# Kernel optimization log

Hardware: AMD Instinct MI355X
Metric: run time of the kernel (lower is better)

The kernel has to match this reference:

```python
import jax, jax.numpy as jnp
import numpy as np

D_MODEL = 1024
N_HEADS = 16
D_K = D_MODEL // N_HEADS


def setup_inputs() -> dict:
    key = jax.random.key(0)
    ks = jax.random.split(key, 5)
    x = jax.random.normal(ks[0], (4, 2048, D_MODEL), dtype=jnp.float32)
    # nn.Linear stores weight as [out, in]; we store transposed [in, out] for x @ W
    w_qkv = jax.random.normal(ks[1], (D_MODEL, 3 * D_MODEL), dtype=jnp.float32) / np.sqrt(D_MODEL)
    b_qkv = jnp.zeros((3 * D_MODEL,), dtype=jnp.float32)
    w_fc = jax.random.normal(ks[2], (D_MODEL, D_MODEL), dtype=jnp.float32) / np.sqrt(D_MODEL)
    b_fc = jnp.zeros((D_MODEL,), dtype=jnp.float32)
    ln_g = jnp.ones((D_MODEL,), dtype=jnp.float32)
    ln_b = jnp.zeros((D_MODEL,), dtype=jnp.float32)
    return {"x": x, "w_qkv": w_qkv, "b_qkv": b_qkv, "w_fc": w_fc, "b_fc": b_fc,
            "ln_g": ln_g, "ln_b": ln_b}


def _layernorm(x, g, b, eps=1e-5):
    mu = jnp.mean(x, axis=-1, keepdims=True)
    var = jnp.mean(jnp.square(x - mu), axis=-1, keepdims=True)
    return (x - mu) * jax.lax.rsqrt(var + eps) * g + b


def reference(x, w_qkv, b_qkv, w_fc, b_fc, ln_g, ln_b):
    residual = x
    xn = _layernorm(x, ln_g, ln_b)
    B, L, D = xn.shape
    qkv = xn @ w_qkv + b_qkv  # [B, L, 3D]
    q, k, v = jnp.split(qkv, 3, axis=-1)
    # b l (h d) -> b h l d
    def to_heads(t):
        return t.reshape(B, L, N_HEADS, D_K).transpose(0, 2, 1, 3)
    q, k, v = to_heads(q), to_heads(k), to_heads(v)
    scale = 1.0 / np.sqrt(D_K)
    scores = jnp.einsum('bhld,bhmd->bhlm', q, k) * scale  # [B,H,L,L]
    attn = jax.nn.softmax(scores, axis=-1)
    # dropout is identity in eval mode
    out = jnp.einsum('bhlm,bhmd->bhld', attn, v)  # [B,H,L,d]
    out = out.transpose(0, 2, 1, 3).reshape(B, L, D)  # b h l d -> b l (h d)
    out = out @ w_fc + b_fc
    return out + residual
```

## Files before the change

kernel.cpp:

```cpp
#include <hip/hip_runtime.h>
#include <hip/hip_bf16.h>
#include <cstdint>
#include <cstddef>

using bf16 = __hip_bfloat16;
typedef __attribute__((ext_vector_type(4))) float f32x4;
typedef __attribute__((ext_vector_type(8))) short bf16x8;

#define D_MODEL 1024
#define SEQ     2048
#define NB      4
#define NHEAD   16
#define DHEAD   64
#define NROWS   (NB * SEQ)

__device__ __forceinline__ void load_lds16(const void* g, void* l) {
  __builtin_amdgcn_global_load_lds(
      (const __attribute__((address_space(1))) unsigned int*)g,
      (__attribute__((address_space(3))) unsigned int*)l, 16, 0, 0);
}

__device__ __forceinline__ unsigned short f2bf(float f) {
  bf16 h = __float2bfloat16(f);
  return *(unsigned short*)&h;
}

__device__ __forceinline__ unsigned pk_trunc(float a, float b) {
  union { float f; unsigned u; } ca, cb;
  ca.f = a; cb.f = b;
  return (ca.u >> 16) | (cb.u & 0xffff0000u);
}

__global__ __launch_bounds__(256) void ln_kernel(
    const float* __restrict__ x, const float* __restrict__ g,
    const float* __restrict__ bb, bf16* __restrict__ xn) {
  int row  = blockIdx.x * 4 + (threadIdx.x >> 6);
  int lane = threadIdx.x & 63;
  const float4* xr = (const float4*)(x + (size_t)row * D_MODEL);
  float v[16], s = 0.f;
#pragma unroll
  for (int i = 0; i < 4; i++) {
    float4 t = xr[lane + 64 * i];
    v[4 * i] = t.x; v[4 * i + 1] = t.y; v[4 * i + 2] = t.z; v[4 * i + 3] = t.w;
    s += t.x + t.y + t.z + t.w;
  }
#pragma unroll
  for (int off = 32; off; off >>= 1) s += __shfl_xor(s, off, 64);
  float mean = s * (1.f / D_MODEL);
  float vs = 0.f;
#pragma unroll
  for (int i = 0; i < 16; i++) { float d = v[i] - mean; vs += d * d; }
#pragma unroll
  for (int off = 32; off; off >>= 1) vs += __shfl_xor(vs, off, 64);
  float rstd = rsqrtf(vs * (1.f / D_MODEL) + 1e-5f);
  ushort4* op = (ushort4*)(xn + (size_t)row * D_MODEL);
#pragma unroll
  for (int i = 0; i < 4; i++) {
    float4 gv = ((const float4*)g)[lane + 64 * i];
    float4 bv = ((const float4*)bb)[lane + 64 * i];
    ushort4 o;
    o.x = f2bf((v[4 * i]     - mean) * rstd * gv.x + bv.x);
    o.y = f2bf((v[4 * i + 1] - mean) * rstd * gv.y + bv.y);
    o.z = f2bf((v[4 * i + 2] - mean) * rstd * gv.z + bv.z);
    o.w = f2bf((v[4 * i + 3] - mean) * rstd * gv.w + bv.w);
    op[lane + 64 * i] = o;
  }
}

__global__ __launch_bounds__(256) void transpose_kernel(
    const float* __restrict__ w_qkv, bf16* __restrict__ wqkvT,
    const float* __restrict__ w_fc, bf16* __restrict__ wfcT) {
  __shared__ float tile[32][33];
  const float* in; bf16* out; int C, c0;
  if (blockIdx.x < 96) { in = w_qkv; out = wqkvT; C = 3072; c0 = blockIdx.x * 32; }
  else                 { in = w_fc;  out = wfcT;  C = 1024; c0 = (blockIdx.x - 96) * 32; }
  int r0 = blockIdx.y * 32;
  int tx = threadIdx.x & 31, ty = threadIdx.x >> 5;
  for (int i = ty; i < 32; i += 8)
    tile[i][tx] = in[(size_t)(r0 + i) * C + c0 + tx];
  __syncthreads();
  for (int i = ty; i < 32; i += 8)
    out[(size_t)(c0 + i) * 1024 + r0 + tx] = __float2bfloat16(tile[tx][i]);
}

__device__ __forceinline__ void store_ct(bf16* p, float v)  { *p = __float2bfloat16(v); }
__device__ __forceinline__ void store_ct(float* p, float v) { *p = v; }

template <int SPLIT, int RESID, typename CT>
__global__ __launch_bounds__(256) void gemm_bt(
    const bf16* __restrict__ A, const bf16* __restrict__ Bt,
    const float* __restrict__ bias, const float* __restrict__ resid,
    CT* __restrict__ C, bf16* __restrict__ vt, int M, int N, int K) {
  __shared__ __attribute__((aligned(16))) bf16 Alds[128 * 64];
  __shared__ __attribute__((aligned(16))) bf16 Blds[128 * 64];
  int tid = threadIdx.x, wave = tid >> 6, lane = tid & 63;
  int ntiles = N >> 7;
  int bm = blockIdx.x / ntiles, bn = blockIdx.x % ntiles;
  int m0 = bm << 7, n0 = bn << 7;
  int wm = (wave >> 1) << 6, wn = (wave & 1) << 6;
  int srow = tid >> 3;
  int sw8  = (((tid & 7) ^ (srow & 7)) << 3);
  int frow = lane & 15, quad = lane >> 4;
  const bf16* Ap[4];
  const bf16* Bp[4];
#pragma unroll
  for (int s = 0; s < 4; s++) {
    Ap[s] = A  + (size_t)(m0 + s * 32 + srow) * K + sw8;
    Bp[s] = Bt + (size_t)(n0 + s * 32 + srow) * K + sw8;
  }
  f32x4 acc[4][4] = {};
  for (int k0 = 0; k0 < K; k0 += 64) {
    __syncthreads();
#pragma unroll
    for (int s = 0; s < 4; s++) {
      load_lds16(Ap[s], (char*)Alds + s * 4096 + tid * 16);
      load_lds16(Bp[s], (char*)Blds + s * 4096 + tid * 16);
      Ap[s] += 64; Bp[s] += 64;
    }
    __syncthreads();
    bf16x8 af[4][2], bv[4][2];
#pragma unroll
    for (int i = 0; i < 4; i++)
#pragma unroll
      for (int kk = 0; kk < 2; kk++) {
        int e = (((kk * 4 + quad) ^ (frow & 7)) << 3);
        af[i][kk] = *(const bf16x8*)&Alds[(wm + i * 16 + frow) * 64 + e];
        bv[i][kk] = *(const bf16x8*)&Blds[(wn + i * 16 + frow) * 64 + e];
      }
#pragma unroll
    for (int i = 0; i < 4; i++)
#pragma unroll
      for (int j = 0; j < 4; j++) {
        acc[i][j] = __builtin_amdgcn_mfma_f32_16x16x32_bf16(af[i][0], bv[j][0], acc[i][j], 0, 0, 0);
        acc[i][j] = __builtin_amdgcn_mfma_f32_16x16x32_bf16(af[i][1], bv[j][1], acc[i][j], 0, 0, 0);
      }
  }
#pragma unroll
  for (int i = 0; i < 4; i++) {
    int row0 = m0 + wm + i * 16 + (quad << 2);
#pragma unroll
    for (int j = 0; j < 4; j++) {
      int col = n0 + wn + j * 16 + frow;
      float bvs = bias[col];
      if (SPLIT && col >= 2048) {
        int hd = col - 2048;
        int b = row0 >> 11, seq0 = row0 & 2047;
        int within = seq0 & 63, mt = within >> 4, q4 = (within >> 2) & 3;
        int pos = (seq0 & ~63) + ((mt >> 1) << 5) + (q4 << 3) + ((mt & 1) << 2);
        ushort4 pk;
        pk.x = f2bf(acc[i][j][0] + bvs);
        pk.y = f2bf(acc[i][j][1] + bvs);
        pk.z = f2bf(acc[i][j][2] + bvs);
        pk.w = f2bf(acc[i][j][3] + bvs);
        *(ushort4*)&vt[((size_t)(b * 1024 + hd)) * SEQ + pos] = pk;
      } else {
        int stride = SPLIT ? 2048 : N;
        float scale = (SPLIT && col < 1024) ? 0.18033688f : 1.0f;
#pragma unroll
        for (int r = 0; r < 4; r++) {
          size_t idx = (size_t)(row0 + r) * stride + col;
          float val = (acc[i][j][r] + bvs) * scale;
          if (RESID) val += resid[idx];
          store_ct(&C[idx], val);
        }
      }
    }
  }
}


template <bool STG>
__device__ __forceinline__ void ktile_qkv(
    const bf16* Aw, const bf16* Bw,
    bf16* Ad, bf16* Bd,
    const bf16* const* Ab, const bf16* const* Bb, size_t koff,
    int tid, int frow, int e_lo, int e_hi, f32x4 (&acc)[8][3]) {
  __builtin_amdgcn_sched_barrier(0);
  bf16x8 bv[3][2];
#pragma unroll
  for (int j = 0; j < 3; j++) {
    bv[j][0] = *(const bf16x8*)&Bw[(j * 16 + frow) * 64 + e_lo];
    bv[j][1] = *(const bf16x8*)&Bw[(j * 16 + frow) * 64 + e_hi];
  }
  bf16x8 a00 = *(const bf16x8*)&Aw[(frow) * 64 + e_lo];
  bf16x8 a01 = *(const bf16x8*)&Aw[(frow) * 64 + e_hi];
  bf16x8 a10 = *(const bf16x8*)&Aw[(16 + frow) * 64 + e_lo];
  bf16x8 a11 = *(const bf16x8*)&Aw[(16 + frow) * 64 + e_hi];
  if (STG) {
#pragma unroll
    for (int u = 0; u < 4; u++)
      load_lds16(Ab[u] + koff, (char*)Ad + u * 8192 + tid * 16);
#pragma unroll
    for (int u = 0; u < 3; u++)
      load_lds16(Bb[u] + koff, (char*)Bd + u * 8192 + tid * 16);
  }
  __builtin_amdgcn_s_barrier();
  asm volatile("s_waitcnt lgkmcnt(0)" ::: "memory");
  __builtin_amdgcn_sched_barrier(0);
  __builtin_amdgcn_s_setprio(1);
#pragma unroll
  for (int j = 0; j < 3; j++) {
    acc[0][j] = __builtin_amdgcn_mfma_f32_16x16x32_bf16(a00, bv[j][0], acc[0][j], 0, 0, 0);
    acc[0][j] = __builtin_amdgcn_mfma_f32_16x16x32_bf16(a01, bv[j][1], acc[0][j], 0, 0, 0);
    acc[1][j] = __builtin_amdgcn_mfma_f32_16x16x32_bf16(a10, bv[j][0], acc[1][j], 0, 0, 0);
    acc[1][j] = __builtin_amdgcn_mfma_f32_16x16x32_bf16(a11, bv[j][1], acc[1][j], 0, 0, 0);
  }
  __builtin_amdgcn_s_setprio(0);
  __builtin_amdgcn_s_barrier();
#pragma unroll
  for (int p = 1; p < 4; p++) {
    bf16x8 c00 = *(const bf16x8*)&Aw[((2 * p) * 16 + frow) * 64 + e_lo];
    bf16x8 c01 = *(const bf16x8*)&Aw[((2 * p) * 16 + frow) * 64 + e_hi];
    bf16x8 c10 = *(const bf16x8*)&Aw[((2 * p + 1) * 16 + frow) * 64 + e_lo];
    bf16x8 c11 = *(const bf16x8*)&Aw[((2 * p + 1) * 16 + frow) * 64 + e_hi];
    __builtin_amdgcn_s_barrier();
    asm volatile("s_waitcnt lgkmcnt(0)" ::: "memory");
    __builtin_amdgcn_sched_barrier(0);
    __builtin_amdgcn_s_setprio(1);
#pragma unroll
    for (int j = 0; j < 3; j++) {
      acc[2 * p][j]     = __builtin_amdgcn_mfma_f32_16x16x32_bf16(c00, bv[j][0], acc[2 * p][j], 0, 0, 0);
      acc[2 * p][j]     = __builtin_amdgcn_mfma_f32_16x16x32_bf16(c01, bv[j][1], acc[2 * p][j], 0, 0, 0);
      acc[2 * p + 1][j] = __builtin_amdgcn_mfma_f32_16x16x32_bf16(c10, bv[j][0], acc[2 * p + 1][j], 0, 0, 0);
      acc[2 * p + 1][j] = __builtin_amdgcn_mfma_f32_16x16x32_bf16(c11, bv[j][1], acc[2 * p + 1][j], 0, 0, 0);
    }
    __builtin_amdgcn_s_setprio(0);
    if (p == 3) {
      asm volatile("s_waitcnt vmcnt(0)" ::: "memory");
      __builtin_amdgcn_sched_barrier(0);
    }
    __builtin_amdgcn_s_barrier();
  }
}

__global__ __launch_bounds__(512, 2) void gemm256_qkv(
    const bf16* __restrict__ A, const bf16* __restrict__ Bt,
    const float* __restrict__ bias, bf16* __restrict__ C, bf16* __restrict__ vt) {
  __shared__ __attribute__((aligned(16))) bf16 AL0[256 * 64];
  __shared__ __attribute__((aligned(16))) bf16 AL1[256 * 64];
  __shared__ __attribute__((aligned(16))) bf16 BL0[192 * 64];
  __shared__ __attribute__((aligned(16))) bf16 BL1[192 * 64];

  int bid = blockIdx.x;
  int logical = (bid & 7) * 64 + (bid >> 3);
  int bm = logical >> 4;
  int bn = logical & 15;
  int m0 = bm * 256, n0 = bn * 192;

  int tid = threadIdx.x, wave = tid >> 6, lane = tid & 63;
  int wm = (wave >> 2) * 128;
  int wn = (wave & 3) * 48;
  int srow = tid >> 3;
  int sw8 = (((tid & 7) ^ (srow & 7)) << 3);
  int frow = lane & 15, quad = lane >> 4;
  int e_lo = ((quad ^ (frow & 7)) << 3);
  int e_hi = (((4 + quad) ^ (frow & 7)) << 3);

  const bf16* Ab[4];
  const bf16* Bb[3];
#pragma unroll
  for (int u = 0; u < 4; u++) Ab[u] = A + (size_t)(m0 + u * 64 + srow) * 1024 + sw8;
#pragma unroll
  for (int u = 0; u < 3; u++) Bb[u] = Bt + (size_t)(n0 + u * 64 + srow) * 1024 + sw8;

#pragma unroll
  for (int u = 0; u < 4; u++) load_lds16(Ab[u], (char*)AL0 + u * 8192 + tid * 16);
#pragma unroll
  for (int u = 0; u < 3; u++) load_lds16(Bb[u], (char*)BL0 + u * 8192 + tid * 16);
  asm volatile("s_waitcnt vmcnt(0)" ::: "memory");
  __builtin_amdgcn_sched_barrier(0);
  __builtin_amdgcn_s_barrier();

  f32x4 acc[8][3] = {};
  const bf16* A0w = AL0 + wm * 64;
  const bf16* B0w = BL0 + wn * 64;
  const bf16* A1w = AL1 + wm * 64;
  const bf16* B1w = BL1 + wn * 64;

  size_t ko = 64;
#pragma unroll 1
  for (int t2 = 0; t2 < 14; t2 += 2) {
    ktile_qkv<true>(A0w, B0w, AL1, BL1, Ab, Bb, ko,      tid, frow, e_lo, e_hi, acc);
    ktile_qkv<true>(A1w, B1w, AL0, BL0, Ab, Bb, ko + 64, tid, frow, e_lo, e_hi, acc);
    ko += 128;
  }
  ktile_qkv<true >(A0w, B0w, AL1, BL1, Ab, Bb, ko, tid, frow, e_lo, e_hi, acc);
  ktile_qkv<false>(A1w, B1w, AL0, BL0, Ab, Bb, 0,  tid, frow, e_lo, e_hi, acc);

#pragma unroll
  for (int i = 0; i < 8; i++) {
    int row0 = m0 + wm + i * 16 + (quad << 2);
#pragma unroll
    for (int j = 0; j < 3; j++) {
      int col = n0 + wn + j * 16 + frow;
      float bvs = bias[col];
      if (col >= 2048) {
        int hd = col - 2048;
        int b = row0 >> 11, seq0 = row0 & 2047;
        int within = seq0 & 63, mt = within >> 4, q4 = (within >> 2) & 3;
        int pos = (seq0 & ~63) + ((mt >> 1) << 5) + (q4 << 3) + ((mt & 1) << 2);
        ushort4 pk;
        pk.x = f2bf(acc[i][j][0] + bvs);
        pk.y = f2bf(acc[i][j][1] + bvs);
        pk.z = f2bf(acc[i][j][2] + bvs);
        pk.w = f2bf(acc[i][j][3] + bvs);
        *(ushort4*)&vt[((size_t)(b * 1024 + hd)) * SEQ + pos] = pk;
      } else {
        float scale = (col < 1024) ? 0.18033688f : 1.0f;
#pragma unroll
        for (int r = 0; r < 4; r++) {
          size_t idx = (size_t)(row0 + r) * 2048 + col;
          C[idx] = __float2bfloat16((acc[i][j][r] + bvs) * scale);
        }
      }
    }
  }
}


__device__ __forceinline__ void stage_kv(
    const bf16* Kp0, const bf16* Kp1, const bf16* Vp0, const bf16* Vp1,
    bf16* KB, bf16* VB, int tid) {
  load_lds16(Kp0, (char*)KB + tid * 16);
  load_lds16(Kp1, (char*)KB + 4096 + tid * 16);
  load_lds16(Vp0, (char*)VB + tid * 16);
  load_lds16(Vp1, (char*)VB + 4096 + tid * 16);
}

__device__ __forceinline__ void kv_tile(
    const bf16* KL, const bf16* VL, int frow, int e0,
    const bf16x8 (&qf)[2][2], f32x4 (&l4)[2], f32x4 (&o)[4][2]) {
  f32x4 s[4][2] = {};
#pragma unroll
  for (int mt = 0; mt < 4; mt++) {
    bf16x8 af0 = *(const bf16x8*)&KL[(mt * 16 + frow) * 64 + e0];
    bf16x8 af1 = *(const bf16x8*)&KL[(mt * 16 + frow) * 64 + (e0 ^ 32)];
#pragma unroll
    for (int qt2 = 0; qt2 < 2; qt2++) {
      s[mt][qt2] = __builtin_amdgcn_mfma_f32_16x16x32_bf16(af0, qf[qt2][0], s[mt][qt2], 0, 0, 0);
      s[mt][qt2] = __builtin_amdgcn_mfma_f32_16x16x32_bf16(af1, qf[qt2][1], s[mt][qt2], 0, 0, 0);
    }
  }
  uint2 pk[2][4];
#pragma unroll
  for (int qt2 = 0; qt2 < 2; qt2++)
#pragma unroll
    for (int mt = 0; mt < 4; mt++) {
      f32x4 pv;
      pv[0] = __builtin_amdgcn_exp2f(s[mt][qt2][0]);
      pv[1] = __builtin_amdgcn_exp2f(s[mt][qt2][1]);
      pv[2] = __builtin_amdgcn_exp2f(s[mt][qt2][2]);
      pv[3] = __builtin_amdgcn_exp2f(s[mt][qt2][3]);
      l4[qt2] += pv;
      pk[qt2][mt].x = pk_trunc(pv[0], pv[1]);
      pk[qt2][mt].y = pk_trunc(pv[2], pv[3]);
    }
#pragma unroll
  for (int dt = 0; dt < 4; dt++) {
    bf16x8 vf0 = *(const bf16x8*)&VL[(dt * 16 + frow) * 64 + e0];
    bf16x8 vf1 = *(const bf16x8*)&VL[(dt * 16 + frow) * 64 + (e0 ^ 32)];
#pragma unroll
    for (int qt2 = 0; qt2 < 2; qt2++) {
      union { unsigned u[4]; bf16x8 v; } pf0, pf1;
      pf0.u[0] = pk[qt2][0].x; pf0.u[1] = pk[qt2][0].y;
      pf0.u[2] = pk[qt2][1].x; pf0.u[3] = pk[qt2][1].y;
      pf1.u[0] = pk[qt2][2].x; pf1.u[1] = pk[qt2][2].y;
      pf1.u[2] = pk[qt2][3].x; pf1.u[3] = pk[qt2][3].y;
      o[dt][qt2] = __builtin_amdgcn_mfma_f32_16x16x32_bf16(vf0, pf0.v, o[dt][qt2], 0, 0, 0);
      o[dt][qt2] = __builtin_amdgcn_mfma_f32_16x16x32_bf16(vf1, pf1.v, o[dt][qt2], 0, 0, 0);
    }
  }
}

__global__ __launch_bounds__(256, 4) void attn_kernel(
    const bf16* __restrict__ qk, const bf16* __restrict__ vt,
    bf16* __restrict__ aout) {
  int bh = blockIdx.x;
  int qt = blockIdx.y;
  int bb = bh >> 4, h = bh & 15;
  const bf16* Qg = qk + (size_t)bb * SEQ * 2048 + h * DHEAD;
  const bf16* Kg = Qg + D_MODEL;
  const bf16* Vg = vt + (size_t)bh * DHEAD * SEQ;

  __shared__ __attribute__((aligned(16))) bf16 Qlds[128 * 64];
  __shared__ __attribute__((aligned(16))) bf16 Klds[64 * 64];
  __shared__ __attribute__((aligned(16))) bf16 Vlds[64 * 64];

  int tid = threadIdx.x, wave = tid >> 6, lane = tid & 63;
  int prow = tid >> 3, pch = tid & 7;
  int lch8 = ((pch ^ (prow & 7)) << 3);
  int frow = lane & 15, quad = lane >> 4;
  int e0 = ((quad ^ (frow & 7)) << 3);
  int q0 = qt * 128;

  bf16* K0 = Klds;  bf16* V0 = Vlds;
  bf16* K1 = Qlds;  bf16* V1 = Qlds + 64 * 64;

  const bf16* Kp0 = Kg + (size_t)prow * 2048 + lch8;
  const bf16* Kp1 = Kg + (size_t)(32 + prow) * 2048 + lch8;
  const bf16* Vp0 = Vg + (size_t)prow * SEQ + lch8;
  const bf16* Vp1 = Vg + (size_t)(32 + prow) * SEQ + lch8;
  const size_t KT = (size_t)1 << 17;

#pragma unroll
  for (int s2 = 0; s2 < 4; s2++)
    load_lds16(Qg + (size_t)(q0 + s2 * 32 + prow) * 2048 + lch8,
               (char*)Qlds + s2 * 4096 + tid * 16);
  __syncthreads();
  bf16x8 qf[2][2];
#pragma unroll
  for (int qt2 = 0; qt2 < 2; qt2++)
#pragma unroll
    for (int kk = 0; kk < 2; kk++)
      qf[qt2][kk] =
          *(const bf16x8*)&Qlds[(wave * 32 + qt2 * 16 + frow) * 64 + (e0 ^ (kk * 32))];
  stage_kv(Kp0, Kp1, Vp0, Vp1, K0, V0, tid);
  __syncthreads();

  f32x4 l4[2] = {};
  f32x4 o[4][2] = {};

#pragma unroll 1
  for (int kt = 0; kt < 30; kt += 2) {
    stage_kv(Kp0 + KT, Kp1 + KT, Vp0 + 64, Vp1 + 64, K1, V1, tid);
    kv_tile(K0, V0, frow, e0, qf, l4, o);
    __syncthreads();
    stage_kv(Kp0 + 2 * KT, Kp1 + 2 * KT, Vp0 + 128, Vp1 + 128, K0, V0, tid);
    kv_tile(K1, V1, frow, e0, qf, l4, o);
    __syncthreads();
    Kp0 += 2 * KT; Kp1 += 2 * KT; Vp0 += 128; Vp1 += 128;
  }
  stage_kv(Kp0 + KT, Kp1 + KT, Vp0 + 64, Vp1 + 64, K1, V1, tid);
  kv_tile(K0, V0, frow, e0, qf, l4, o);
  __syncthreads();
  kv_tile(K1, V1, frow, e0, qf, l4, o);

  float linv[2];
#pragma unroll
  for (int qt2 = 0; qt2 < 2; qt2++) {
    float v = (l4[qt2][0] + l4[qt2][1]) + (l4[qt2][2] + l4[qt2][3]);
    v += __shfl_xor(v, 16, 64);
    v += __shfl_xor(v, 32, 64);
    linv[qt2] = 1.f / v;
  }

  __syncthreads();
  bf16* Tw = (wave == 0) ? Qlds
           : (wave == 1) ? Qlds + 32 * 80
           : (wave == 2) ? Klds : Vlds;
#pragma unroll
  for (int qt2 = 0; qt2 < 2; qt2++)
#pragma unroll
    for (int dt = 0; dt < 4; dt++) {
      ushort4 pk;
      pk.x = f2bf(o[dt][qt2][0] * linv[qt2]);
      pk.y = f2bf(o[dt][qt2][1] * linv[qt2]);
      pk.z = f2bf(o[dt][qt2][2] * linv[qt2]);
      pk.w = f2bf(o[dt][qt2][3] * linv[qt2]);
      *(ushort4*)&Tw[(qt2 * 16 + frow) * 80 + dt * 16 + quad * 4] = pk;
    }
  int rq = lane >> 1, d0 = (lane & 1) * 32;
  size_t grow = (size_t)(bb * SEQ + q0 + wave * 32 + rq);
#pragma unroll
  for (int i = 0; i < 4; i++) {
    bf16x8 v8 = *(const bf16x8*)&Tw[rq * 80 + d0 + i * 8];
    *(bf16x8*)&aout[grow * D_MODEL + h * DHEAD + d0 + i * 8] = v8;
  }
}

extern "C" void kernel_launch(void* const* d_in, const int* in_sizes, int n_in,
                              void* d_out, int out_size, void* d_ws, size_t ws_size,
                              hipStream_t stream) {
  const float* x     = (const float*)d_in[0];
  const float* w_qkv = (const float*)d_in[1];
  const float* b_qkv = (const float*)d_in[2];
  const float* w_fc  = (const float*)d_in[3];
  const float* b_fc  = (const float*)d_in[4];
  const float* ln_g  = (const float*)d_in[5];
  const float* ln_b  = (const float*)d_in[6];
  float* out = (float*)d_out;

  char* ws = (char*)d_ws;
  bf16* xn    = (bf16*)(ws);
  bf16* wqkvT = (bf16*)(ws + (16u << 20));
  bf16* wfcT  = (bf16*)(ws + (22u << 20));
  bf16* qk    = (bf16*)(ws + (24u << 20));
  bf16* vt    = (bf16*)(ws + (56u << 20));
  bf16* aout  = (bf16*)(ws);

  ln_kernel<<<NROWS / 4, 256, 0, stream>>>(x, ln_g, ln_b, xn);
  transpose_kernel<<<dim3(128, 32), 256, 0, stream>>>(w_qkv, wqkvT, w_fc, wfcT);
  gemm256_qkv<<<512, 512, 0, stream>>>(xn, wqkvT, b_qkv, qk, vt);
  attn_kernel<<<dim3(NB * NHEAD, SEQ / 128), 256, 0, stream>>>(qk, vt, aout);
  gemm_bt<0, 1, float><<<(NROWS / 128) * (D_MODEL / 128), 256, 0, stream>>>(
      aout, wfcT, b_fc, x, out, nullptr, NROWS, D_MODEL, D_MODEL);
}
```

Before: 270.7 us.

## Replace FC GEMM with 8-wave double-buffered kernel and split QKV staging waits

The simple single-buffered 128x128 output-projection GEMM is replaced by a 512-thread, 256x128-tile kernel. It reuses the templated double-buffered k-tile routine from the QKV GEMM, with an XCD-aware block remap. The shared k-tile routine now issues half of the A-tile prefetch mid-tile and uses partial vmcnt waits instead of a full drain, so global-to-LDS loads overlap more with MFMA work. This risks incorrect synchronisation if the vmcnt counts do not match the load ordering. The FC grid also shrinks to 256 blocks, which may leave CUs underused.

```diff
diff --git a/kernel.cpp b/kernel.cpp
--- a/kernel.cpp
+++ b/kernel.cpp
@@ -83,102 +83,16 @@
     out[(size_t)(c0 + i) * 1024 + r0 + tx] = __float2bfloat16(tile[tx][i]);
 }
 
-__device__ __forceinline__ void store_ct(bf16* p, float v)  { *p = __float2bfloat16(v); }
-__device__ __forceinline__ void store_ct(float* p, float v) { *p = v; }
-
-template <int SPLIT, int RESID, typename CT>
-__global__ __launch_bounds__(256) void gemm_bt(
-    const bf16* __restrict__ A, const bf16* __restrict__ Bt,
-    const float* __restrict__ bias, const float* __restrict__ resid,
-    CT* __restrict__ C, bf16* __restrict__ vt, int M, int N, int K) {
-  __shared__ __attribute__((aligned(16))) bf16 Alds[128 * 64];
-  __shared__ __attribute__((aligned(16))) bf16 Blds[128 * 64];
-  int tid = threadIdx.x, wave = tid >> 6, lane = tid & 63;
-  int ntiles = N >> 7;
-  int bm = blockIdx.x / ntiles, bn = blockIdx.x % ntiles;
-  int m0 = bm << 7, n0 = bn << 7;
-  int wm = (wave >> 1) << 6, wn = (wave & 1) << 6;
-  int srow = tid >> 3;
-  int sw8  = (((tid & 7) ^ (srow & 7)) << 3);
-  int frow = lane & 15, quad = lane >> 4;
-  const bf16* Ap[4];
-  const bf16* Bp[4];
-#pragma unroll
-  for (int s = 0; s < 4; s++) {
-    Ap[s] = A  + (size_t)(m0 + s * 32 + srow) * K + sw8;
-    Bp[s] = Bt + (size_t)(n0 + s * 32 + srow) * K + sw8;
-  }
-  f32x4 acc[4][4] = {};
-  for (int k0 = 0; k0 < K; k0 += 64) {
-    __syncthreads();
-#pragma unroll
-    for (int s = 0; s < 4; s++) {
-      load_lds16(Ap[s], (char*)Alds + s * 4096 + tid * 16);
-      load_lds16(Bp[s], (char*)Blds + s * 4096 + tid * 16);
-      Ap[s] += 64; Bp[s] += 64;
-    }
-    __syncthreads();
-    bf16x8 af[4][2], bv[4][2];
-#pragma unroll
-    for (int i = 0; i < 4; i++)
-#pragma unroll
-      for (int kk = 0; kk < 2; kk++) {
-        int e = (((kk * 4 + quad) ^ (frow & 7)) << 3);
-        af[i][kk] = *(const bf16x8*)&Alds[(wm + i * 16 + frow) * 64 + e];
-        bv[i][kk] = *(const bf16x8*)&Blds[(wn + i * 16 + frow) * 64 + e];
-      }
-#pragma unroll
-    for (int i = 0; i < 4; i++)
-#pragma unroll
-      for (int j = 0; j < 4; j++) {
-        acc[i][j] = __builtin_amdgcn_mfma_f32_16x16x32_bf16(af[i][0], bv[j][0], acc[i][j], 0, 0, 0);
-        acc[i][j] = __builtin_amdgcn_mfma_f32_16x16x32_bf16(af[i][1], bv[j][1], acc[i][j], 0, 0, 0);
-      }
-  }
-#pragma unroll
-  for (int i = 0; i < 4; i++) {
-    int row0 = m0 + wm + i * 16 + (quad << 2);
-#pragma unroll
-    for (int j = 0; j < 4; j++) {
-      int col = n0 + wn + j * 16 + frow;
-      float bvs = bias[col];
-      if (SPLIT && col >= 2048) {
-        int hd = col - 2048;
-        int b = row0 >> 11, seq0 = row0 & 2047;
-        int within = seq0 & 63, mt = within >> 4, q4 = (within >> 2) & 3;
-        int pos = (seq0 & ~63) + ((mt >> 1) << 5) + (q4 << 3) + ((mt & 1) << 2);
-        ushort4 pk;
-        pk.x = f2bf(acc[i][j][0] + bvs);
-        pk.y = f2bf(acc[i][j][1] + bvs);
-        pk.z = f2bf(acc[i][j][2] + bvs);
-        pk.w = f2bf(acc[i][j][3] + bvs);
-        *(ushort4*)&vt[((size_t)(b * 1024 + hd)) * SEQ + pos] = pk;
-      } else {
-        int stride = SPLIT ? 2048 : N;
-        float scale = (SPLIT && col < 1024) ? 0.18033688f : 1.0f;
-#pragma unroll
-        for (int r = 0; r < 4; r++) {
-          size_t idx = (size_t)(row0 + r) * stride + col;
-          float val = (acc[i][j][r] + bvs) * scale;
-          if (RESID) val += resid[idx];
-          store_ct(&C[idx], val);
-        }
-      }
-    }
-  }
-}
-
-
-template <bool STG>
-__device__ __forceinline__ void ktile_qkv(
+template <int BCH, bool STG, bool LAST>
+__device__ __forceinline__ void ktile8(
     const bf16* Aw, const bf16* Bw,
     bf16* Ad, bf16* Bd,
-    const bf16* const* Ab, const bf16* const* Bb, size_t koff,
-    int tid, int frow, int e_lo, int e_hi, f32x4 (&acc)[8][3]) {
+    const bf16* const (&Ab)[4], const bf16* const (&Bb)[BCH], size_t koff,
+    int tid, int frow, int e_lo, int e_hi, f32x4 (&acc)[8][BCH]) {
   __builtin_amdgcn_sched_barrier(0);
-  bf16x8 bv[3][2];
-#pragma unroll
-  for (int j = 0; j < 3; j++) {
+  bf16x8 bv[BCH][2];
+#pragma unroll
+  for (int j = 0; j < BCH; j++) {
     bv[j][0] = *(const bf16x8*)&Bw[(j * 16 + frow) * 64 + e_lo];
     bv[j][1] = *(const bf16x8*)&Bw[(j * 16 + frow) * 64 + e_hi];
   }
@@ -188,18 +102,18 @@
   bf16x8 a11 = *(const bf16x8*)&Aw[(16 + frow) * 64 + e_hi];
   if (STG) {
 #pragma unroll
-    for (int u = 0; u < 4; u++)
-      load_lds16(Ab[u] + koff, (char*)Ad + u * 8192 + tid * 16);
-#pragma unroll
-    for (int u = 0; u < 3; u++)
+    for (int u = 0; u < BCH; u++)
       load_lds16(Bb[u] + koff, (char*)Bd + u * 8192 + tid * 16);
+    load_lds16(Ab[0] + koff, (char*)Ad + tid * 16);
+    load_lds16(Ab[2] + koff, (char*)Ad + 2 * 8192 + tid * 16);
+    __builtin_amdgcn_sched_barrier(0);
   }
   __builtin_amdgcn_s_barrier();
   asm volatile("s_waitcnt lgkmcnt(0)" ::: "memory");
   __builtin_amdgcn_sched_barrier(0);
   __builtin_amdgcn_s_setprio(1);
 #pragma unroll
-  for (int j = 0; j < 3; j++) {
+  for (int j = 0; j < BCH; j++) {
     acc[0][j] = __builtin_amdgcn_mfma_f32_16x16x32_bf16(a00, bv[j][0], acc[0][j], 0, 0, 0);
     acc[0][j] = __builtin_amdgcn_mfma_f32_16x16x32_bf16(a01, bv[j][1], acc[0][j], 0, 0, 0);
     acc[1][j] = __builtin_amdgcn_mfma_f32_16x16x32_bf16(a10, bv[j][0], acc[1][j], 0, 0, 0);
@@ -213,27 +127,38 @@
     bf16x8 c01 = *(const bf16x8*)&Aw[((2 * p) * 16 + frow) * 64 + e_hi];
     bf16x8 c10 = *(const bf16x8*)&Aw[((2 * p + 1) * 16 + frow) * 64 + e_lo];
     bf16x8 c11 = *(const bf16x8*)&Aw[((2 * p + 1) * 16 + frow) * 64 + e_hi];
+    if (STG && p == 2) {
+      load_lds16(Ab[1] + koff, (char*)Ad + 1 * 8192 + tid * 16);
+      load_lds16(Ab[3] + koff, (char*)Ad + 3 * 8192 + tid * 16);
+      __builtin_amdgcn_sched_barrier(0);
+    }
     __builtin_amdgcn_s_barrier();
     asm volatile("s_waitcnt lgkmcnt(0)" ::: "memory");
     __builtin_amdgcn_sched_barrier(0);
     __builtin_amdgcn_s_setprio(1);
 #pragma unroll
-    for (int j = 0; j < 3; j++) {
+    for (int j = 0; j < BCH; j++) {
       acc[2 * p][j]     = __builtin_amdgcn_mfma_f32_16x16x32_bf16(c00, bv[j][0], acc[2 * p][j], 0, 0, 0);
       acc[2 * p][j]     = __builtin_amdgcn_mfma_f32_16x16x32_bf16(c01, bv[j][1], acc[2 * p][j], 0, 0, 0);
       acc[2 * p + 1][j] = __builtin_amdgcn_mfma_f32_16x16x32_bf16(c10, bv[j][0], acc[2 * p + 1][j], 0, 0, 0);
       acc[2 * p + 1][j] = __builtin_amdgcn_mfma_f32_16x16x32_bf16(c11, bv[j][1], acc[2 * p + 1][j], 0, 0, 0);
     }
     __builtin_amdgcn_s_setprio(0);
-    if (p == 3) {
-      asm volatile("s_waitcnt vmcnt(0)" ::: "memory");
+    if (p == 1) {
+      if (LAST) asm volatile("s_waitcnt vmcnt(0)" ::: "memory");
+      else if (BCH == 3) asm volatile("s_waitcnt vmcnt(5)" ::: "memory");
+      else               asm volatile("s_waitcnt vmcnt(4)" ::: "memory");
       __builtin_amdgcn_sched_barrier(0);
     }
+    if (p == 3 && !LAST) {
+      asm volatile("s_waitcnt vmcnt(2)" ::: "memory");
+      __builtin_amdgcn_sched_barrier(0);
+    }
     __builtin_amdgcn_s_barrier();
   }
 }
 
-__global__ __launch_bounds__(512, 2) void gemm256_qkv(
+__global__ __launch_bounds__(512, 2) void gemm8_qkv(
     const bf16* __restrict__ A, const bf16* __restrict__ Bt,
     const float* __restrict__ bias, bf16* __restrict__ C, bf16* __restrict__ vt) {
   __shared__ __attribute__((aligned(16))) bf16 AL0[256 * 64];
@@ -243,13 +168,11 @@
 
   int bid = blockIdx.x;
   int logical = (bid & 7) * 64 + (bid >> 3);
-  int bm = logical >> 4;
-  int bn = logical & 15;
+  int bm = logical >> 4, bn = logical & 15;
   int m0 = bm * 256, n0 = bn * 192;
 
   int tid = threadIdx.x, wave = tid >> 6, lane = tid & 63;
-  int wm = (wave >> 2) * 128;
-  int wn = (wave & 3) * 48;
+  int wm = (wave >> 2) * 128, wn = (wave & 3) * 48;
   int srow = tid >> 3;
   int sw8 = (((tid & 7) ^ (srow & 7)) << 3);
   int frow = lane & 15, quad = lane >> 4;
@@ -264,9 +187,9 @@
   for (int u = 0; u < 3; u++) Bb[u] = Bt + (size_t)(n0 + u * 64 + srow) * 1024 + sw8;
 
 #pragma unroll
+  for (int u = 0; u < 3; u++) load_lds16(Bb[u], (char*)BL0 + u * 8192 + tid * 16);
+#pragma unroll
   for (int u = 0; u < 4; u++) load_lds16(Ab[u], (char*)AL0 + u * 8192 + tid * 16);
-#pragma unroll
-  for (int u = 0; u < 3; u++) load_lds16(Bb[u], (char*)BL0 + u * 8192 + tid * 16);
   asm volatile("s_waitcnt vmcnt(0)" ::: "memory");
   __builtin_amdgcn_sched_barrier(0);
   __builtin_amdgcn_s_barrier();
@@ -279,13 +202,13 @@
 
   size_t ko = 64;
 #pragma unroll 1
-  for (int t2 = 0; t2 < 14; t2 += 2) {
-    ktile_qkv<true>(A0w, B0w, AL1, BL1, Ab, Bb, ko,      tid, frow, e_lo, e_hi, acc);
-    ktile_qkv<true>(A1w, B1w, AL0, BL0, Ab, Bb, ko + 64, tid, frow, e_lo, e_hi, acc);
+  for (int t2 = 0; t2 < 7; t2++) {
+    ktile8<3, true, false>(A0w, B0w, AL1, BL1, Ab, Bb, ko,      tid, frow, e_lo, e_hi, acc);
+    ktile8<3, true, false>(A1w, B1w, AL0, BL0, Ab, Bb, ko + 64, tid, frow, e_lo, e_hi, acc);
     ko += 128;
   }
-  ktile_qkv<true >(A0w, B0w, AL1, BL1, Ab, Bb, ko, tid, frow, e_lo, e_hi, acc);
-  ktile_qkv<false>(A1w, B1w, AL0, BL0, Ab, Bb, 0,  tid, frow, e_lo, e_hi, acc);
+  ktile8<3, true,  false>(A0w, B0w, AL1, BL1, Ab, Bb, ko, tid, frow, e_lo, e_hi, acc);
+  ktile8<3, false, true >(A1w, B1w, AL0, BL0, Ab, Bb, 0,  tid, frow, e_lo, e_hi, acc);
 
 #pragma unroll
   for (int i = 0; i < 8; i++) {
@@ -317,6 +240,75 @@
   }
 }
 
+__global__ __launch_bounds__(512, 2) void gemm8_fc(
+    const bf16* __restrict__ A, const bf16* __restrict__ Bt,
+    const float* __restrict__ bias, const float* __restrict__ resid,
+    float* __restrict__ out) {
+  __shared__ __attribute__((aligned(16))) bf16 AL0[256 * 64];
+  __shared__ __attribute__((aligned(16))) bf16 AL1[256 * 64];
+  __shared__ __attribute__((aligned(16))) bf16 BL0[128 * 64];
+  __shared__ __attribute__((aligned(16))) bf16 BL1[128 * 64];
+
+  int bid = blockIdx.x;
+  int logical = (bid & 7) * 32 + (bid >> 3);
+  int bm = logical >> 3, bn = logical & 7;
+  int m0 = bm * 256, n0 = bn * 128;
+
+  int tid = threadIdx.x, wave = tid >> 6, lane = tid & 63;
+  int wm = (wave >> 2) * 128, wn = (wave & 3) * 32;
+  int srow = tid >> 3;
+  int sw8 = (((tid & 7) ^ (srow & 7)) << 3);
+  int frow = lane & 15, quad = lane >> 4;
+  int e_lo = ((quad ^ (frow & 7)) << 3);
+  int e_hi = (((4 + quad) ^ (frow & 7)) << 3);
+
+  const bf16* Ab[4];
+  const bf16* Bb[2];
+#pragma unroll
+  for (int u = 0; u < 4; u++) Ab[u] = A + (size_t)(m0 + u * 64 + srow) * 1024 + sw8;
+#pragma unroll
+  for (int u = 0; u < 2; u++) Bb[u] = Bt + (size_t)(n0 + u * 64 + srow) * 1024 + sw8;
+
+#pragma unroll
+  for (int u = 0; u < 2; u++) load_lds16(Bb[u], (char*)BL0 + u * 8192 + tid * 16);
+#pragma unroll
+  for (int u = 0; u < 4; u++) load_lds16(Ab[u], (char*)AL0 + u * 8192 + tid * 16);
+  asm volatile("s_waitcnt vmcnt(0)" ::: "memory");
+  __builtin_amdgcn_sched_barrier(0);
+  __builtin_amdgcn_s_barrier();
+
+  f32x4 acc[8][2] = {};
+  const bf16* A0w = AL0 + wm * 64;
+  const bf16* B0w = BL0 + wn * 64;
+  const bf16* A1w = AL1 + wm * 64;
+  const bf16* B1w = BL1 + wn * 64;
+
+  size_t ko = 64;
+#pragma unroll 1
+  for (int t2 = 0; t2 < 7; t2++) {
+    ktile8<2, true, false>(A0w, B0w, AL1, BL1, Ab, Bb, ko,      tid, frow, e_lo, e_hi, acc);
+    ktile8<2, true, false>(A1w, B1w, AL0, BL0, Ab, Bb, ko + 64, tid, frow, e_lo, e_hi, acc);
+    ko += 128;
+  }
+  ktile8<2, true,  false>(A0w, B0w, AL1, BL1, Ab, Bb, ko, tid, frow, e_lo, e_hi, acc);
+  ktile8<2, false, true >(A1w, B1w, AL0, BL0, Ab, Bb, 0,  tid, frow, e_lo, e_hi, acc);
+
+#pragma unroll
+  for (int i = 0; i < 8; i++) {
+    int row0 = m0 + wm + i * 16 + (quad << 2);
+#pragma unroll
+    for (int j = 0; j < 2; j++) {
+      int col = n0 + wn + j * 16 + frow;
+      float bvs = bias[col];
+#pragma unroll
+      for (int r = 0; r < 4; r++) {
+        size_t idx = (size_t)(row0 + r) * 1024 + col;
+        out[idx] = (acc[i][j][r] + bvs) + resid[idx];
+      }
+    }
+  }
+}
+
 
 __device__ __forceinline__ void stage_kv(
     const bf16* Kp0, const bf16* Kp1, const bf16* Vp0, const bf16* Vp1,
@@ -490,8 +482,7 @@
 
   ln_kernel<<<NROWS / 4, 256, 0, stream>>>(x, ln_g, ln_b, xn);
   transpose_kernel<<<dim3(128, 32), 256, 0, stream>>>(w_qkv, wqkvT, w_fc, wfcT);
-  gemm256_qkv<<<512, 512, 0, stream>>>(xn, wqkvT, b_qkv, qk, vt);
+  gemm8_qkv<<<512, 512, 0, stream>>>(xn, wqkvT, b_qkv, qk, vt);
   attn_kernel<<<dim3(NB * NHEAD, SEQ / 128), 256, 0, stream>>>(qk, vt, aout);
-  gemm_bt<0, 1, float><<<(NROWS / 128) * (D_MODEL / 128), 256, 0, stream>>>(
-      aout, wfcT, b_fc, x, out, nullptr, NROWS, D_MODEL, D_MODEL);
-}
+  gemm8_fc<<<256, 512, 0, stream>>>(aout, wfcT, b_fc, x, out);
+}
```

Measured after the change: 270.1 us. Within noise of the previous version (-0.2%).
